# Kernel optimization log

Hardware: AMD Instinct MI355X
Metric: run time of the kernel (lower is better)

Reference implementation:

```python
import jax, jax.numpy as jnp
import numpy as np
from jax import lax

B, T, D, H, K = 2, 2048, 1024, 16, 4
HD = D // H           # head dim = 64
CONV_DIM = 3 * D      # q + k + v channels


def _l2norm(x, eps=1e-6):
    return x * lax.rsqrt(jnp.sum(x * x, axis=-1, keepdims=True) + eps)


def setup_inputs() -> dict:
    key = jax.random.key(0)
    ks = jax.random.split(key, 8)
    s = 0.02
    return {
        "x": jax.random.normal(ks[0], (B, T, D), jnp.float32),
        "W_qkv": jax.random.normal(ks[1], (CONV_DIM, D), jnp.float32) * s,
        "conv_w": jax.random.normal(ks[2], (CONV_DIM, 1, K), jnp.float32) * 0.25,
        "W_z": jax.random.normal(ks[3], (D, D), jnp.float32) * s,
        "W_b": jax.random.normal(ks[4], (H, D), jnp.float32) * s,
        "W_a": jax.random.normal(ks[5], (H, D), jnp.float32) * s,
        "dt_bias": jnp.ones((H,), jnp.float32),
        "A_log": jnp.log(jnp.arange(1, H + 1, dtype=jnp.float32)),
        "W_out": jax.random.normal(ks[6], (D, D), jnp.float32) * s,
    }


def _forward(x, W_qkv, conv_w, W_z, W_b, W_a, dt_bias, A_log, W_out):
    b_, t_, d_ = x.shape
    # fused qkv projection: [B,T,3D]
    mixed = jnp.einsum("btd,cd->btc", x, W_qkv)
    # causal depthwise conv1d (left pad K-1, truncate to T)
    c = mixed.transpose(0, 2, 1)  # [B,3D,T]
    c = lax.conv_general_dilated(
        c, conv_w, window_strides=(1,), padding=[(K - 1, 0)],
        dimension_numbers=("NCH", "OIH", "NCH"), feature_group_count=CONV_DIM)
    mixed = jax.nn.silu(c).transpose(0, 2, 1)  # [B,T,3D]

    q, k, v = jnp.split(mixed, [d_, 2 * d_], axis=-1)
    q = q.reshape(b_, t_, H, HD)
    k = k.reshape(b_, t_, H, HD)
    v = v.reshape(b_, t_, H, HD)

    z = jnp.einsum("btd,ed->bte", x, W_z).reshape(b_, t_, H, HD)
    beta = jax.nn.sigmoid(jnp.einsum("btd,hd->bth", x, W_b))          # [B,T,H]
    g = -jnp.exp(A_log) * jax.nn.softplus(
        jnp.einsum("btd,hd->bth", x, W_a) + dt_bias)                   # [B,T,H]

    q = _l2norm(q) * (HD ** -0.5)
    k = _l2norm(k)

    # sequential gated delta-rule scan over time
    qs = q.transpose(1, 0, 2, 3)       # [T,B,H,HD]
    ks_ = k.transpose(1, 0, 2, 3)
    vs = v.transpose(1, 0, 2, 3)
    bs = beta.transpose(1, 0, 2)       # [T,B,H]
    gs = g.transpose(1, 0, 2)

    def step(S, inp):
        q_t, k_t, v_t, b_t, g_t = inp
        S = S * jnp.exp(g_t)[..., None, None]                         # decay state
        S = S + jnp.einsum("bhd,bhv->bhdv", k_t, v_t * b_t[..., None])  # rank-1 update
        o_t = jnp.einsum("bhd,bhdv->bhv", q_t, S)
        return S, o_t

    S0 = jnp.zeros((b_, H, HD, HD), x.dtype)
    _, out = lax.scan(step, S0, (qs, ks_, vs, bs, gs))                 # out: [T,B,H,HD]
    out = out.transpose(1, 0, 2, 3)                                    # [B,T,H,HD]

    # gated RMSNorm over head dim, gate = silu(z)
    var = jnp.mean(out * out, axis=-1, keepdims=True)
    out = out * lax.rsqrt(var + 1e-6) * jax.nn.silu(z)

    out = out.reshape(b_, t_, d_)
    return jnp.einsum("btd,ed->bte", out, W_out)


def reference(x, W_qkv, conv_w, W_z, W_b, W_a, dt_bias, A_log, W_out):
    return _forward(x, W_qkv, conv_w, W_z, W_b, W_a, dt_bias, A_log, W_out)
```

## Files before the change

kernel.cpp:

```cpp
#include <hip/hip_runtime.h>
#include <math.h>

#define B_  2
#define T_  2048
#define D_  1024
#define H_  16
#define HD_ 64
#define CD_ 3072
#define L_  64
#define NC_ 32
#define TS  72
#define TT  8

typedef __attribute__((ext_vector_type(8))) short bf16x8;
typedef __attribute__((ext_vector_type(4))) float f32x4;
typedef __attribute__((ext_vector_type(4))) unsigned short u16x4;

__device__ __forceinline__ unsigned short f2bf(float f) {
    unsigned int u = __float_as_uint(f);
    unsigned int r = (u + 0x7fffu + ((u >> 16) & 1u)) >> 16;
    return (unsigned short)r;
}
__device__ __forceinline__ float bf2f(unsigned short u) {
    return __uint_as_float(((unsigned int)u) << 16);
}

__global__ __launch_bounds__(256)
void cvt_all(const float* __restrict__ x, const float* __restrict__ Wqkv,
             const float* __restrict__ Wz, const float* __restrict__ Wout,
             unsigned short* __restrict__ xb, unsigned short* __restrict__ Wqkvb,
             unsigned short* __restrict__ Wzb, unsigned short* __restrict__ Woutb) {
    int i = blockIdx.x * 256 + threadIdx.x;
    const float* src; unsigned short* dst; int li;
    if (i < 1048576)      { src = x;    dst = xb;    li = i; }
    else if (i < 1835008) { src = Wqkv; dst = Wqkvb; li = i - 1048576; }
    else if (i < 2097152) { src = Wz;   dst = Wzb;   li = i - 1835008; }
    else                  { src = Wout; dst = Woutb; li = i - 2097152; }
    float4 a = ((const float4*)src)[li];
    u16x4 o;
    o.x = f2bf(a.x); o.y = f2bf(a.y); o.z = f2bf(a.z); o.w = f2bf(a.w);
    ((u16x4*)dst)[li] = o;
}

__global__ __launch_bounds__(512, 2)
void gemm_qkvz256(const unsigned short* __restrict__ A,
                  const unsigned short* __restrict__ Bw,
                  unsigned short* __restrict__ mixedb, unsigned short* __restrict__ zb) {
    const int K = 1024;
    extern __shared__ short lds[];
    const int tid = threadIdx.x;
    const int bm = (blockIdx.x >> 4) * 256;
    const int bn = (blockIdx.x & 15) * 256;
    const int wid = tid >> 6;
    const int lane = tid & 63;
    const int wm = (wid >> 2) * 128;
    const int wn = (wid & 3) * 64;
    const int lr = lane & 15;
    const int lk = lane >> 4;

    f32x4 acc[8][4] = {};

    const int srow = tid >> 3;
    const int sphys = tid & 7;
    const int sgcol = ((sphys ^ (srow & 7)) << 3);
    const unsigned short* Ag = A + (size_t)(bm + srow) * K + sgcol;
    const unsigned short* Bg = Bw + (size_t)(bn + srow) * K + sgcol;
    short* ldsAd = lds + srow * 64 + sphys * 8;
    short* ldsBd = ldsAd + 16384;

#define SA2(bsel, kt, j0)                                                        \
    do {                                                                         \
        _Pragma("unroll")                                                        \
        for (int jj = (j0); jj < (j0) + 2; ++jj)                                 \
            __builtin_amdgcn_global_load_lds(                                    \
                (const __attribute__((address_space(1))) void*)(Ag + (size_t)(jj * 64) * K + (kt) * 64), \
                (__attribute__((address_space(3))) void*)(ldsAd + (bsel) * 32768 + jj * 4096), 16, 0, 0); \
    } while (0)
#define SB2(bsel, kt, j0)                                                        \
    do {                                                                         \
        _Pragma("unroll")                                                        \
        for (int jj = (j0); jj < (j0) + 2; ++jj)                                 \
            __builtin_amdgcn_global_load_lds(                                    \
                (const __attribute__((address_space(1))) void*)(Bg + (size_t)(jj * 64) * K + (kt) * 64), \
                (__attribute__((address_space(3))) void*)(ldsBd + (bsel) * 32768 + jj * 4096), 16, 0, 0); \
    } while (0)

    SA2(0, 0, 0); SB2(0, 0, 0); SA2(0, 0, 2); SB2(0, 0, 2);

    for (int kt = 0; kt < 16; ++kt) {
        const int cur = kt & 1;
        const int nb = cur ^ 1;
        asm volatile("s_waitcnt vmcnt(0)" ::: "memory");
        __builtin_amdgcn_sched_barrier(0);
        __builtin_amdgcn_s_barrier();
        const short* LA = lds + cur * 32768 + (wm + lr) * 64;
        const short* LB = lds + cur * 32768 + 16384 + (wn + lr) * 64;
        bf16x8 bf[4], af[4];
        const int ch0 = (lk ^ (lr & 7)) * 8;
        const int ch1 = ((4 + lk) ^ (lr & 7)) * 8;

#pragma unroll
        for (int ni = 0; ni < 4; ++ni) bf[ni] = *(const bf16x8*)(LB + ni * 1024 + ch0);
#pragma unroll
        for (int mi = 0; mi < 4; ++mi) af[mi] = *(const bf16x8*)(LA + mi * 1024 + ch0);
        if (kt < 15) SA2(nb, kt + 1, 0);
        __builtin_amdgcn_s_setprio(1);
#pragma unroll
        for (int mi = 0; mi < 4; ++mi)
#pragma unroll
            for (int ni = 0; ni < 4; ++ni)
                acc[mi][ni] = __builtin_amdgcn_mfma_f32_16x16x32_bf16(
                    af[mi], bf[ni], acc[mi][ni], 0, 0, 0);
        __builtin_amdgcn_s_setprio(0);
        __builtin_amdgcn_s_barrier();

#pragma unroll
        for (int mi = 0; mi < 4; ++mi) af[mi] = *(const bf16x8*)(LA + (mi + 4) * 1024 + ch0);
        if (kt < 15) SB2(nb, kt + 1, 0);
        __builtin_amdgcn_s_setprio(1);
#pragma unroll
        for (int mi = 0; mi < 4; ++mi)
#pragma unroll
            for (int ni = 0; ni < 4; ++ni)
                acc[mi + 4][ni] = __builtin_amdgcn_mfma_f32_16x16x32_bf16(
                    af[mi], bf[ni], acc[mi + 4][ni], 0, 0, 0);
        __builtin_amdgcn_s_setprio(0);
        __builtin_amdgcn_s_barrier();

#pragma unroll
        for (int ni = 0; ni < 4; ++ni) bf[ni] = *(const bf16x8*)(LB + ni * 1024 + ch1);
#pragma unroll
        for (int mi = 0; mi < 4; ++mi) af[mi] = *(const bf16x8*)(LA + mi * 1024 + ch1);
        if (kt < 15) SA2(nb, kt + 1, 2);
        __builtin_amdgcn_s_setprio(1);
#pragma unroll
        for (int mi = 0; mi < 4; ++mi)
#pragma unroll
            for (int ni = 0; ni < 4; ++ni)
                acc[mi][ni] = __builtin_amdgcn_mfma_f32_16x16x32_bf16(
                    af[mi], bf[ni], acc[mi][ni], 0, 0, 0);
        __builtin_amdgcn_s_setprio(0);
        __builtin_amdgcn_s_barrier();

#pragma unroll
        for (int mi = 0; mi < 4; ++mi) af[mi] = *(const bf16x8*)(LA + (mi + 4) * 1024 + ch1);
        if (kt < 15) SB2(nb, kt + 1, 2);
        __builtin_amdgcn_s_setprio(1);
#pragma unroll
        for (int mi = 0; mi < 4; ++mi)
#pragma unroll
            for (int ni = 0; ni < 4; ++ni)
                acc[mi + 4][ni] = __builtin_amdgcn_mfma_f32_16x16x32_bf16(
                    af[mi], bf[ni], acc[mi + 4][ni], 0, 0, 0);
        __builtin_amdgcn_s_setprio(0);
        __builtin_amdgcn_s_barrier();
    }

    const int r0 = lk * 4;
#pragma unroll
    for (int mi = 0; mi < 8; ++mi)
#pragma unroll
        for (int ni = 0; ni < 4; ++ni) {
            int row = bm + wm + mi * 16 + r0;
            int col = bn + wn + ni * 16 + lr;
            if (bn < 3072) {
                unsigned short* cp = mixedb + (size_t)row * 3072 + col;
#pragma unroll
                for (int r = 0; r < 4; ++r) cp[(size_t)r * 3072] = f2bf(acc[mi][ni][r]);
            } else {
                unsigned short* cp = zb + (size_t)row * 1024 + (col - 3072);
#pragma unroll
                for (int r = 0; r < 4; ++r) cp[(size_t)r * 1024] = f2bf(acc[mi][ni][r]);
            }
        }
}

__global__ __launch_bounds__(256, 2)
void gemm_out(const unsigned short* __restrict__ A,
              const unsigned short* __restrict__ Bw,
              float* __restrict__ C) {
    const int K = 1024, N = 1024;
    __shared__ short Ls[2][16384];
    const int tid = threadIdx.x;
    const int bm = (blockIdx.x >> 3) * 128;
    const int bn = (blockIdx.x & 7) * 128;
    const int wave = tid >> 6;
    const int lane = tid & 63;
    const int wm = (wave >> 1) * 64;
    const int wn = (wave & 1) * 64;
    const int lr = lane & 15;
    const int lk = lane >> 4;

    f32x4 acc[4][4] = {};

    const int srow = tid >> 3;
    const int sphys = tid & 7;
    const int sgcol = ((sphys ^ (srow & 7)) << 3);
    const unsigned short* Ag = A + (size_t)(bm + srow) * K + sgcol;
    const unsigned short* Bg = Bw + (size_t)(bn + srow) * K + sgcol;
    short* ldsAd = &Ls[0][0] + srow * 64 + sphys * 8;
    short* ldsBd = ldsAd + 8192;

#define STG_O(bsel, kt)                                                          \
    do {                                                                         \
        _Pragma("unroll")                                                        \
        for (int j = 0; j < 4; ++j) {                                            \
            __builtin_amdgcn_global_load_lds(                                    \
                (const __attribute__((address_space(1))) void*)(Ag + (size_t)(j * 32) * K + (kt) * 64), \
                (__attribute__((address_space(3))) void*)(ldsAd + (bsel) * 16384 + j * 2048), 16, 0, 0); \
            __builtin_amdgcn_global_load_lds(                                    \
                (const __attribute__((address_space(1))) void*)(Bg + (size_t)(j * 32) * K + (kt) * 64), \
                (__attribute__((address_space(3))) void*)(ldsBd + (bsel) * 16384 + j * 2048), 16, 0, 0); \
        }                                                                        \
    } while (0)

#define CMP_O(bsel)                                                              \
    do {                                                                         \
        const short* LA = &Ls[bsel][0] + (wm + lr) * 64;                         \
        const short* LB = &Ls[bsel][8192] + (wn + lr) * 64;                      \
        _Pragma("unroll")                                                        \
        for (int ks = 0; ks < 2; ++ks) {                                         \
            const int ch = ((ks * 4 + lk) ^ (lr & 7)) * 8;                       \
            bf16x8 af[4], bf[4];                                                 \
            _Pragma("unroll")                                                    \
            for (int mi = 0; mi < 4; ++mi) af[mi] = *(const bf16x8*)(LA + mi * 1024 + ch); \
            _Pragma("unroll")                                                    \
            for (int ni = 0; ni < 4; ++ni) bf[ni] = *(const bf16x8*)(LB + ni * 1024 + ch); \
            __builtin_amdgcn_s_setprio(1);                                       \
            _Pragma("unroll")                                                    \
            for (int mi = 0; mi < 4; ++mi)                                       \
                _Pragma("unroll")                                                \
                for (int ni = 0; ni < 4; ++ni)                                   \
                    acc[mi][ni] = __builtin_amdgcn_mfma_f32_16x16x32_bf16(       \
                        af[mi], bf[ni], acc[mi][ni], 0, 0, 0);                   \
            __builtin_amdgcn_s_setprio(0);                                       \
        }                                                                        \
    } while (0)

    STG_O(0, 0);
    __syncthreads();
    for (int kt = 0; kt < 15; ++kt) {
        STG_O((kt + 1) & 1, kt + 1);
        CMP_O(kt & 1);
        __syncthreads();
    }
    CMP_O(1);

    const int r0 = lk * 4;
#pragma unroll
    for (int mi = 0; mi < 4; ++mi)
#pragma unroll
        for (int ni = 0; ni < 4; ++ni) {
            float* cp = C + (size_t)(bm + wm + mi * 16 + r0) * N + bn + wn + ni * 16 + lr;
#pragma unroll
            for (int r = 0; r < 4; ++r)
                cp[(size_t)r * N] = acc[mi][ni][r];
        }
}

#define PJS 129
__global__ __launch_bounds__(256)
void proj_bg_partial(const float* __restrict__ x, const float* __restrict__ Wb,
                     const float* __restrict__ Wa, float* __restrict__ partial) {
    const int m0 = (blockIdx.x >> 3) * 32;
    const int ks = blockIdx.x & 7;
    const int k0 = ks * 128;
    const int tid = threadIdx.x;
    __shared__ float xs[32 * PJS];
    __shared__ float wsh[32 * PJS];
    const int sr = tid >> 3;
    const int sc = (tid & 7) << 4;
    const int mi2 = tid >> 3;
    const int n02 = (tid & 7) << 2;

    {
        const float* xrow = x + (size_t)(m0 + sr) * D_ + k0 + sc;
        const float* wrow = ((sr < 16) ? (Wb + (size_t)sr * D_) : (Wa + (size_t)(sr - 16) * D_)) + k0 + sc;
#pragma unroll
        for (int j = 0; j < 16; j += 4) {
            float4 a = *(const float4*)(xrow + j);
            float4 b = *(const float4*)(wrow + j);
            xs[sr * PJS + sc + j + 0] = a.x; xs[sr * PJS + sc + j + 1] = a.y;
            xs[sr * PJS + sc + j + 2] = a.z; xs[sr * PJS + sc + j + 3] = a.w;
            wsh[sr * PJS + sc + j + 0] = b.x; wsh[sr * PJS + sc + j + 1] = b.y;
            wsh[sr * PJS + sc + j + 2] = b.z; wsh[sr * PJS + sc + j + 3] = b.w;
        }
    }
    __syncthreads();

    float acc[4] = {0.f, 0.f, 0.f, 0.f};
#pragma unroll 8
    for (int kk = 0; kk < 128; ++kk) {
        float av = xs[mi2 * PJS + kk];
#pragma unroll
        for (int j = 0; j < 4; ++j)
            acc[j] = fmaf(av, wsh[(n02 + j) * PJS + kk], acc[j]);
    }
    float* op = partial + (size_t)ks * (4096 * 32) + (size_t)(m0 + mi2) * 32 + n02;
    *(float4*)op = make_float4(acc[0], acc[1], acc[2], acc[3]);
}

__global__ __launch_bounds__(256)
void proj_bg_reduce(const float* __restrict__ partial, const float* __restrict__ dt_bias,
                    const float* __restrict__ A_log,
                    float* __restrict__ beta, float* __restrict__ g) {
    const int gid = blockIdx.x * 256 + threadIdx.x;
    const int m = gid >> 5;
    const int n = gid & 31;
    float s = 0.f;
#pragma unroll
    for (int ks = 0; ks < 8; ++ks)
        s += partial[(size_t)ks * (4096 * 32) + gid];
    if (n < 16) {
        beta[(size_t)m * H_ + n] = 1.f / (1.f + expf(-s));
    } else {
        int h = n - 16;
        float spin = s + dt_bias[h];
        float sp = (spin > 20.f) ? spin : log1pf(expf(spin));
        g[(size_t)m * H_ + h] = -expf(A_log[h]) * sp;
    }
}

__global__ __launch_bounds__(256)
void conv_silu_tt(const unsigned short* __restrict__ mixedb,
                  const float* __restrict__ conv_w,
                  unsigned short* __restrict__ qkvb) {
    int idx = blockIdx.x * 256 + threadIdx.x;
    const int cq = idx % (CD_ / 4);
    const int bt8 = idx / (CD_ / 4);
    const int t0 = (bt8 % (T_ / TT)) * TT;
    const int b = bt8 / (T_ / TT);
    const int c0 = cq << 2;
    const unsigned short* base = mixedb + (size_t)(b * T_ + t0) * CD_ + c0;

    float vals[TT + 3][4];
#pragma unroll
    for (int i = 0; i < TT + 3; ++i) {
        int t = t0 + i - 3;
        if (t >= 0) {
            u16x4 m = *(const u16x4*)(base + (ptrdiff_t)(i - 3) * CD_);
            vals[i][0] = bf2f(m.x); vals[i][1] = bf2f(m.y);
            vals[i][2] = bf2f(m.z); vals[i][3] = bf2f(m.w);
        } else {
            vals[i][0] = vals[i][1] = vals[i][2] = vals[i][3] = 0.f;
        }
    }
    const float4* wp = (const float4*)(conv_w + (size_t)c0 * 4);
    float4 w[4] = {wp[0], wp[1], wp[2], wp[3]};

    unsigned short* outp = qkvb + (size_t)(b * T_ + t0) * CD_ + c0;
#pragma unroll
    for (int tt = 0; tt < TT; ++tt) {
        u16x4 r;
        float s0 = vals[tt + 3][0] * w[0].w + vals[tt + 2][0] * w[0].z
                 + vals[tt + 1][0] * w[0].y + vals[tt + 0][0] * w[0].x;
        float s1 = vals[tt + 3][1] * w[1].w + vals[tt + 2][1] * w[1].z
                 + vals[tt + 1][1] * w[1].y + vals[tt + 0][1] * w[1].x;
        float s2 = vals[tt + 3][2] * w[2].w + vals[tt + 2][2] * w[2].z
                 + vals[tt + 1][2] * w[2].y + vals[tt + 0][2] * w[2].x;
        float s3 = vals[tt + 3][3] * w[3].w + vals[tt + 2][3] * w[3].z
                 + vals[tt + 1][3] * w[3].y + vals[tt + 0][3] * w[3].x;
        r.x = f2bf(s0 / (1.f + expf(-s0)));
        r.y = f2bf(s1 / (1.f + expf(-s1)));
        r.z = f2bf(s2 / (1.f + expf(-s2)));
        r.w = f2bf(s3 / (1.f + expf(-s3)));
        *(u16x4*)(outp + (size_t)tt * CD_) = r;
    }
}

__global__ __launch_bounds__(256)
void chunk_phase1(const unsigned short* __restrict__ qkvb,
                  const float* __restrict__ beta, const float* __restrict__ gg,
                  float* __restrict__ dST, float* __restrict__ cum,
                  float* __restrict__ ac) {
    const int cid = blockIdx.x;
    const int c = cid & (NC_ - 1);
    const int bh = cid >> 5;
    const int b = bh >> 4, h = bh & 15;
    const int tid = threadIdx.x;
    const int wave = tid >> 6, lane = tid & 63;
    const int t0 = c * L_;

    __shared__ __align__(16) short kT[64 * TS];
    __shared__ __align__(16) short vT[64 * TS];
    __shared__ float cumS[64], wS[64];
    __shared__ float ksumP[4][64];

    const unsigned short* rowp = qkvb + (size_t)(b * T_ + t0 + lane) * CD_ + h * HD_ + wave * 16;
    bf16x8 k0 = *(const bf16x8*)(rowp + D_);
    bf16x8 k1 = *(const bf16x8*)(rowp + D_ + 8);
    bf16x8 v0 = *(const bf16x8*)(rowp + 2 * D_);
    bf16x8 v1 = *(const bf16x8*)(rowp + 2 * D_ + 8);

    {
        float ks = 0.f;
#pragma unroll
        for (int j = 0; j < 8; ++j) {
            float a = bf2f((unsigned short)k0[j]); ks = fmaf(a, a, ks);
            float bq = bf2f((unsigned short)k1[j]); ks = fmaf(bq, bq, ks);
        }
        ksumP[wave][lane] = ks;
    }

    if (wave == 0) {
        float s = gg[(size_t)(b * T_ + t0 + lane) * H_ + h];
#pragma unroll
        for (int off = 1; off < 64; off <<= 1) {
            float up = __shfl_up(s, off, 64);
            if (lane >= off) s += up;
        }
        cumS[lane] = s;
        float cend = __shfl(s, 63, 64);
        wS[lane] = expf(cend - s) * beta[(size_t)(b * T_ + t0 + lane) * H_ + h];
        cum[(size_t)bh * T_ + t0 + lane] = s;
        if (lane == 63) ac[cid] = expf(cend);
    }
    __syncthreads();
    const float kn = rsqrtf(ksumP[0][lane] + ksumP[1][lane] + ksumP[2][lane]
                            + ksumP[3][lane] + 1e-6f);
    const float w = wS[lane] * kn;
#pragma unroll
    for (int j = 0; j < 8; ++j) {
        kT[(wave * 16 + j) * TS + lane] = k0[j];
        kT[(wave * 16 + 8 + j) * TS + lane] = k1[j];
        vT[(wave * 16 + j) * TS + lane] = f2bf(bf2f((unsigned short)v0[j]) * w);
        vT[(wave * 16 + 8 + j) * TS + lane] = f2bf(bf2f((unsigned short)v1[j]) * w);
    }
    __syncthreads();

    const int lr = lane & 15, lk = lane >> 4;
    f32x4 acc[4] = {};
    const short* pA = vT + (wave * 16 + lr) * TS + lk * 8;
#pragma unroll
    for (int kk = 0; kk < 2; ++kk) {
        bf16x8 a = *(const bf16x8*)(pA + kk * 32);
#pragma unroll
        for (int n = 0; n < 4; ++n) {
            bf16x8 bfr = *(const bf16x8*)(kT + (n * 16 + lr) * TS + lk * 8 + kk * 32);
            acc[n] = __builtin_amdgcn_mfma_f32_16x16x32_bf16(a, bfr, acc[n], 0, 0, 0);
        }
    }
#pragma unroll
    for (int n = 0; n < 4; ++n) {
        float* op = dST + (size_t)cid * 4096 + (wave * 16 + lk * 4) * 64 + n * 16 + lr;
#pragma unroll
        for (int r = 0; r < 4; ++r)
            op[r * 64] = acc[n][r];
    }
}

__global__ __launch_bounds__(256)
void chunk_phase2(float* __restrict__ dST, const float* __restrict__ ac) {
    const int gid = blockIdx.x * 256 + threadIdx.x;
    const int bh = gid >> 12;
    const int e = gid & 4095;
    float s = 0.f;
    for (int c = 0; c < NC_; ++c) {
        size_t off = (size_t)(bh * NC_ + c) * 4096 + e;
        float tmp = dST[off];
        dST[off] = s;
        s = fmaf(ac[bh * NC_ + c], s, tmp);
    }
}

__global__ __launch_bounds__(256)
void chunk_phase3(const unsigned short* __restrict__ qkvb,
                  const float* __restrict__ beta, const float* __restrict__ cum,
                  const float* __restrict__ states,
                  const unsigned short* __restrict__ zb,
                  unsigned short* __restrict__ normb) {
    const int cid = blockIdx.x;
    const int c = cid & (NC_ - 1);
    const int bh = cid >> 5;
    const int b = bh >> 4, h = bh & 15;
    const int tid = threadIdx.x;
    const int wave = tid >> 6, lane = tid & 63;
    const int t0 = c * L_;

    __shared__ __align__(16) short vT[64 * TS];
    __shared__ __align__(16) short sT[64 * TS];
    __shared__ __align__(16) short pS[64 * TS];
    __shared__ float cumS[64], betaS[64];
    __shared__ float invq[64], invk[64];

    {
        const unsigned short* rowp = qkvb + (size_t)(b * T_ + t0 + lane) * CD_ + 2 * D_ + h * HD_ + wave * 16;
        bf16x8 v0 = *(const bf16x8*)rowp;
        bf16x8 v1 = *(const bf16x8*)(rowp + 8);
#pragma unroll
        for (int j = 0; j < 8; ++j) {
            vT[(wave * 16 + j) * TS + lane] = v0[j];
            vT[(wave * 16 + 8 + j) * TS + lane] = v1[j];
        }
    }
    {
        const float* sp = states + (size_t)cid * 4096 + (tid >> 2) * 64 + (tid & 3) * 16;
        short* dp = sT + (tid >> 2) * TS + (tid & 3) * 16;
#pragma unroll
        for (int j = 0; j < 16; j += 4) {
            float4 f = *(const float4*)(sp + j);
            dp[j] = f2bf(f.x); dp[j + 1] = f2bf(f.y);
            dp[j + 2] = f2bf(f.z); dp[j + 3] = f2bf(f.w);
        }
    }
    {
        int row = tid >> 2;
        int seg = (tid & 3) << 4;
        const unsigned short* qr = qkvb + (size_t)(b * T_ + t0 + row) * CD_ + h * HD_ + seg;
        bf16x8 a0 = *(const bf16x8*)qr;
        bf16x8 a1 = *(const bf16x8*)(qr + 8);
        float sq = 0.f;
#pragma unroll
        for (int j = 0; j < 8; ++j) {
            float v = bf2f((unsigned short)a0[j]); sq = fmaf(v, v, sq);
            v = bf2f((unsigned short)a1[j]); sq = fmaf(v, v, sq);
        }
        sq += __shfl_xor(sq, 1, 64);
        sq += __shfl_xor(sq, 2, 64);
        const unsigned short* kr = qr + D_;
        bf16x8 b0 = *(const bf16x8*)kr;
        bf16x8 b1 = *(const bf16x8*)(kr + 8);
        float sk = 0.f;
#pragma unroll
        for (int j = 0; j < 8; ++j) {
            float v = bf2f((unsigned short)b0[j]); sk = fmaf(v, v, sk);
            v = bf2f((unsigned short)b1[j]); sk = fmaf(v, v, sk);
        }
        sk += __shfl_xor(sk, 1, 64);
        sk += __shfl_xor(sk, 2, 64);
        if ((tid & 3) == 0) {
            invq[row] = 0.125f * rsqrtf(sq + 1e-6f);
            invk[row] = rsqrtf(sk + 1e-6f);
        }
    }
    if (tid < 64) {
        cumS[tid] = cum[(size_t)bh * T_ + t0 + tid];
        betaS[tid] = beta[(size_t)(b * T_ + t0 + tid) * H_ + h];
    }
    __syncthreads();

    const int lr = lane & 15, lk = lane >> 4;
    const unsigned short* qrow = qkvb + (size_t)(b * T_ + t0 + wave * 16 + lr) * CD_ + h * HD_;
    bf16x8 qf0 = *(const bf16x8*)(qrow + lk * 8);
    bf16x8 qf1 = *(const bf16x8*)(qrow + 32 + lk * 8);

    f32x4 pacc[4] = {};
#pragma unroll
    for (int n = 0; n < 4; ++n) {
        const unsigned short* krow = qkvb + (size_t)(b * T_ + t0 + n * 16 + lr) * CD_ + D_ + h * HD_;
        bf16x8 b0 = *(const bf16x8*)(krow + lk * 8);
        bf16x8 b1 = *(const bf16x8*)(krow + 32 + lk * 8);
        pacc[n] = __builtin_amdgcn_mfma_f32_16x16x32_bf16(qf0, b0, pacc[n], 0, 0, 0);
        pacc[n] = __builtin_amdgcn_mfma_f32_16x16x32_bf16(qf1, b1, pacc[n], 0, 0, 0);
    }
#pragma unroll
    for (int n = 0; n < 4; ++n) {
        int s = n * 16 + lr;
        float cs = cumS[s], bsk = betaS[s] * invk[s];
#pragma unroll
        for (int r = 0; r < 4; ++r) {
            int t = wave * 16 + lk * 4 + r;
            float pv = (s <= t) ? expf(cumS[t] - cs) * bsk * pacc[n][r] * invq[t] : 0.f;
            pS[t * TS + s] = f2bf(pv);
        }
    }
    __syncthreads();

    f32x4 oacc[4] = {};
#pragma unroll
    for (int n = 0; n < 4; ++n) {
        const short* srow = sT + (n * 16 + lr) * TS + lk * 8;
        bf16x8 b0 = *(const bf16x8*)srow;
        bf16x8 b1 = *(const bf16x8*)(srow + 32);
        oacc[n] = __builtin_amdgcn_mfma_f32_16x16x32_bf16(qf0, b0, oacc[n], 0, 0, 0);
        oacc[n] = __builtin_amdgcn_mfma_f32_16x16x32_bf16(qf1, b1, oacc[n], 0, 0, 0);
    }
    float qsc[4];
#pragma unroll
    for (int r = 0; r < 4; ++r) {
        int t = wave * 16 + lk * 4 + r;
        qsc[r] = expf(cumS[t]) * invq[t];
    }
#pragma unroll
    for (int n = 0; n < 4; ++n)
#pragma unroll
        for (int r = 0; r < 4; ++r) oacc[n][r] *= qsc[r];
    const short* prow = pS + (wave * 16 + lr) * TS + lk * 8;
    bf16x8 pf0 = *(const bf16x8*)prow;
    bf16x8 pf1 = *(const bf16x8*)(prow + 32);
#pragma unroll
    for (int n = 0; n < 4; ++n) {
        const short* vrow = vT + (n * 16 + lr) * TS + lk * 8;
        bf16x8 b0 = *(const bf16x8*)vrow;
        bf16x8 b1 = *(const bf16x8*)(vrow + 32);
        oacc[n] = __builtin_amdgcn_mfma_f32_16x16x32_bf16(pf0, b0, oacc[n], 0, 0, 0);
        oacc[n] = __builtin_amdgcn_mfma_f32_16x16x32_bf16(pf1, b1, oacc[n], 0, 0, 0);
    }

#pragma unroll
    for (int r = 0; r < 4; ++r) {
        int t = wave * 16 + lk * 4 + r;
        float ss = 0.f;
#pragma unroll
        for (int n = 0; n < 4; ++n) ss = fmaf(oacc[n][r], oacc[n][r], ss);
        ss += __shfl_xor(ss, 1, 64);
        ss += __shfl_xor(ss, 2, 64);
        ss += __shfl_xor(ss, 4, 64);
        ss += __shfl_xor(ss, 8, 64);
        float inv = rsqrtf(ss * (1.f / 64.f) + 1e-6f);
        size_t rowoff = (size_t)(b * T_ + t0 + t) * D_ + h * HD_;
#pragma unroll
        for (int n = 0; n < 4; ++n) {
            float zv = bf2f(zb[rowoff + n * 16 + lr]);
            float sz = zv / (1.f + expf(-zv));
            normb[rowoff + n * 16 + lr] = f2bf(oacc[n][r] * inv * sz);
        }
    }
}

extern "C" void kernel_launch(void* const* d_in, const int* in_sizes, int n_in,
                              void* d_out, int out_size, void* d_ws, size_t ws_size,
                              hipStream_t stream) {
    const float* x       = (const float*)d_in[0];
    const float* W_qkv   = (const float*)d_in[1];
    const float* conv_w  = (const float*)d_in[2];
    const float* W_z     = (const float*)d_in[3];
    const float* W_b     = (const float*)d_in[4];
    const float* W_a     = (const float*)d_in[5];
    const float* dt_bias = (const float*)d_in[6];
    const float* A_log   = (const float*)d_in[7];
    const float* W_out   = (const float*)d_in[8];
    float* out = (float*)d_out;

    float* ws = (float*)d_ws;
    unsigned short* mixedb = (unsigned short*)ws;
    float* dST    = ws;
    unsigned short* normb = (unsigned short*)(ws + 4194304);
    float* betab  = ws + 8388608;
    float* gb     = ws + 8454144;
    float* cum    = ws + 8519680;
    float* ac     = ws + 8585216;
    unsigned short* Woutb = (unsigned short*)(ws + 8586240);
    unsigned short* xb    = (unsigned short*)(ws + 12582912);
    unsigned short* Wqkvb = (unsigned short*)(ws + 14680064);
    unsigned short* Wzb   = (unsigned short*)(ws + 16252928);
    unsigned short* qkvb  = (unsigned short*)(ws + 12582912);
    unsigned short* zb    = (unsigned short*)(ws + 18874368);
    float* bgpart = ws + 23068672;

    const int M = B_ * T_;
    dim3 blk(256);

    cvt_all<<<dim3(9216), blk, 0, stream>>>(x, W_qkv, W_z, W_out, xb, Wqkvb, Wzb, Woutb);

    gemm_qkvz256<<<dim3(256), dim3(512), 131072, stream>>>(xb, Wqkvb, mixedb, zb);

    conv_silu_tt<<<dim3(B_ * (T_ / TT) * (CD_ / 4) / 256), blk, 0, stream>>>(mixedb, conv_w, qkvb);

    proj_bg_partial<<<dim3(1024), blk, 0, stream>>>(x, W_b, W_a, bgpart);
    proj_bg_reduce<<<dim3(512), blk, 0, stream>>>(bgpart, dt_bias, A_log, betab, gb);

    chunk_phase1<<<dim3(B_ * H_ * NC_), blk, 0, stream>>>(qkvb, betab, gb, dST, cum, ac);
    chunk_phase2<<<dim3(B_ * H_ * 4096 / 256), blk, 0, stream>>>(dST, ac);
    chunk_phase3<<<dim3(B_ * H_ * NC_), blk, 0, stream>>>(qkvb, betab, cum, dST, zb, normb);

    gemm_out<<<dim3(256), blk, 0, stream>>>(normb, Woutb, out);
}
```

Before: 134.0 us.

## Fuse causal conv+SiLU and beta/g reduction into chunk phase kernels

Removes the standalone conv_silu_tt and proj_bg_reduce kernels. Chunk phase1 and phase3 now load the raw projected rows, compute the depthwise causal conv and SiLU on the fly, and phase1 also reduces the beta/g partial sums itself. Phase3 stages q and k in shared memory and computes the norms from them. This drops two launches and the round trip of the qkv intermediate through global memory. In exchange, conv work is recomputed in both phases and each output row now needs four input rows of loads. The workspace layout is reshuffled to fit.

```diff
diff --git a/kernel.cpp b/kernel.cpp
--- a/kernel.cpp
+++ b/kernel.cpp
@@ -10,7 +10,6 @@
 #define L_  64
 #define NC_ 32
 #define TS  72
-#define TT  8
 
 typedef __attribute__((ext_vector_type(8))) short bf16x8;
 typedef __attribute__((ext_vector_type(4))) float f32x4;
@@ -301,78 +300,12 @@
 }
 
 __global__ __launch_bounds__(256)
-void proj_bg_reduce(const float* __restrict__ partial, const float* __restrict__ dt_bias,
-                    const float* __restrict__ A_log,
-                    float* __restrict__ beta, float* __restrict__ g) {
-    const int gid = blockIdx.x * 256 + threadIdx.x;
-    const int m = gid >> 5;
-    const int n = gid & 31;
-    float s = 0.f;
-#pragma unroll
-    for (int ks = 0; ks < 8; ++ks)
-        s += partial[(size_t)ks * (4096 * 32) + gid];
-    if (n < 16) {
-        beta[(size_t)m * H_ + n] = 1.f / (1.f + expf(-s));
-    } else {
-        int h = n - 16;
-        float spin = s + dt_bias[h];
-        float sp = (spin > 20.f) ? spin : log1pf(expf(spin));
-        g[(size_t)m * H_ + h] = -expf(A_log[h]) * sp;
-    }
-}
-
-__global__ __launch_bounds__(256)
-void conv_silu_tt(const unsigned short* __restrict__ mixedb,
+void chunk_phase1(const unsigned short* __restrict__ mixedb,
                   const float* __restrict__ conv_w,
-                  unsigned short* __restrict__ qkvb) {
-    int idx = blockIdx.x * 256 + threadIdx.x;
-    const int cq = idx % (CD_ / 4);
-    const int bt8 = idx / (CD_ / 4);
-    const int t0 = (bt8 % (T_ / TT)) * TT;
-    const int b = bt8 / (T_ / TT);
-    const int c0 = cq << 2;
-    const unsigned short* base = mixedb + (size_t)(b * T_ + t0) * CD_ + c0;
-
-    float vals[TT + 3][4];
-#pragma unroll
-    for (int i = 0; i < TT + 3; ++i) {
-        int t = t0 + i - 3;
-        if (t >= 0) {
-            u16x4 m = *(const u16x4*)(base + (ptrdiff_t)(i - 3) * CD_);
-            vals[i][0] = bf2f(m.x); vals[i][1] = bf2f(m.y);
-            vals[i][2] = bf2f(m.z); vals[i][3] = bf2f(m.w);
-        } else {
-            vals[i][0] = vals[i][1] = vals[i][2] = vals[i][3] = 0.f;
-        }
-    }
-    const float4* wp = (const float4*)(conv_w + (size_t)c0 * 4);
-    float4 w[4] = {wp[0], wp[1], wp[2], wp[3]};
-
-    unsigned short* outp = qkvb + (size_t)(b * T_ + t0) * CD_ + c0;
-#pragma unroll
-    for (int tt = 0; tt < TT; ++tt) {
-        u16x4 r;
-        float s0 = vals[tt + 3][0] * w[0].w + vals[tt + 2][0] * w[0].z
-                 + vals[tt + 1][0] * w[0].y + vals[tt + 0][0] * w[0].x;
-        float s1 = vals[tt + 3][1] * w[1].w + vals[tt + 2][1] * w[1].z
-                 + vals[tt + 1][1] * w[1].y + vals[tt + 0][1] * w[1].x;
-        float s2 = vals[tt + 3][2] * w[2].w + vals[tt + 2][2] * w[2].z
-                 + vals[tt + 1][2] * w[2].y + vals[tt + 0][2] * w[2].x;
-        float s3 = vals[tt + 3][3] * w[3].w + vals[tt + 2][3] * w[3].z
-                 + vals[tt + 1][3] * w[3].y + vals[tt + 0][3] * w[3].x;
-        r.x = f2bf(s0 / (1.f + expf(-s0)));
-        r.y = f2bf(s1 / (1.f + expf(-s1)));
-        r.z = f2bf(s2 / (1.f + expf(-s2)));
-        r.w = f2bf(s3 / (1.f + expf(-s3)));
-        *(u16x4*)(outp + (size_t)tt * CD_) = r;
-    }
-}
-
-__global__ __launch_bounds__(256)
-void chunk_phase1(const unsigned short* __restrict__ qkvb,
-                  const float* __restrict__ beta, const float* __restrict__ gg,
+                  const float* __restrict__ bgpart,
+                  const float* __restrict__ dt_bias, const float* __restrict__ A_log,
                   float* __restrict__ dST, float* __restrict__ cum,
-                  float* __restrict__ ac) {
+                  float* __restrict__ ac, float* __restrict__ betab) {
     const int cid = blockIdx.x;
     const int c = cid & (NC_ - 1);
     const int bh = cid >> 5;
@@ -386,24 +319,62 @@
     __shared__ float cumS[64], wS[64];
     __shared__ float ksumP[4][64];
 
-    const unsigned short* rowp = qkvb + (size_t)(b * T_ + t0 + lane) * CD_ + h * HD_ + wave * 16;
-    bf16x8 k0 = *(const bf16x8*)(rowp + D_);
-    bf16x8 k1 = *(const bf16x8*)(rowp + D_ + 8);
-    bf16x8 v0 = *(const bf16x8*)(rowp + 2 * D_);
-    bf16x8 v1 = *(const bf16x8*)(rowp + 2 * D_ + 8);
-
-    {
-        float ks = 0.f;
+    const int colk = D_ + h * HD_ + wave * 16;
+    const int tloc = t0 + lane;
+    const bf16x8 zz = {0, 0, 0, 0, 0, 0, 0, 0};
+    bf16x8 kr[4][2], vr[4][2];
+#pragma unroll
+    for (int ri = 0; ri < 4; ++ri) {
+        int tt = tloc - 3 + ri;
+        if (tt >= 0) {
+            const unsigned short* bp = mixedb + (size_t)(b * T_ + tt) * CD_ + colk;
+            kr[ri][0] = *(const bf16x8*)bp;
+            kr[ri][1] = *(const bf16x8*)(bp + 8);
+            vr[ri][0] = *(const bf16x8*)(bp + D_);
+            vr[ri][1] = *(const bf16x8*)(bp + D_ + 8);
+        } else {
+            kr[ri][0] = zz; kr[ri][1] = zz; vr[ri][0] = zz; vr[ri][1] = zz;
+        }
+    }
+    unsigned short kb[16], vb[16];
+    float ksq = 0.f;
+#pragma unroll
+    for (int half = 0; half < 2; ++half)
 #pragma unroll
         for (int j = 0; j < 8; ++j) {
-            float a = bf2f((unsigned short)k0[j]); ks = fmaf(a, a, ks);
-            float bq = bf2f((unsigned short)k1[j]); ks = fmaf(bq, bq, ks);
-        }
-        ksumP[wave][lane] = ks;
-    }
+            int ch = colk + half * 8 + j;
+            float4 wk = *(const float4*)(conv_w + (size_t)ch * 4);
+            float sk = bf2f((unsigned short)kr[3][half][j]) * wk.w
+                     + bf2f((unsigned short)kr[2][half][j]) * wk.z
+                     + bf2f((unsigned short)kr[1][half][j]) * wk.y
+                     + bf2f((unsigned short)kr[0][half][j]) * wk.x;
+            sk = sk / (1.f + expf(-sk));
+            unsigned short kbi = f2bf(sk);
+            kb[half * 8 + j] = kbi;
+            float kf = bf2f(kbi);
+            ksq = fmaf(kf, kf, ksq);
+            float4 wv = *(const float4*)(conv_w + (size_t)(ch + D_) * 4);
+            float sv = bf2f((unsigned short)vr[3][half][j]) * wv.w
+                     + bf2f((unsigned short)vr[2][half][j]) * wv.z
+                     + bf2f((unsigned short)vr[1][half][j]) * wv.y
+                     + bf2f((unsigned short)vr[0][half][j]) * wv.x;
+            sv = sv / (1.f + expf(-sv));
+            vb[half * 8 + j] = f2bf(sv);
+        }
+    ksumP[wave][lane] = ksq;
 
     if (wave == 0) {
-        float s = gg[(size_t)(b * T_ + t0 + lane) * H_ + h];
+        const int m = b * T_ + t0 + lane;
+        float sb = 0.f, sg = 0.f;
+#pragma unroll
+        for (int p = 0; p < 8; ++p) {
+            sb += bgpart[(size_t)p * 131072 + m * 32 + h];
+            sg += bgpart[(size_t)p * 131072 + m * 32 + 16 + h];
+        }
+        float bet = 1.f / (1.f + expf(-sb));
+        float spin = sg + dt_bias[h];
+        float sp = (spin > 20.f) ? spin : log1pf(expf(spin));
+        float s = -expf(A_log[h]) * sp;
 #pragma unroll
         for (int off = 1; off < 64; off <<= 1) {
             float up = __shfl_up(s, off, 64);
@@ -411,8 +382,9 @@
         }
         cumS[lane] = s;
         float cend = __shfl(s, 63, 64);
-        wS[lane] = expf(cend - s) * beta[(size_t)(b * T_ + t0 + lane) * H_ + h];
+        wS[lane] = expf(cend - s) * bet;
         cum[(size_t)bh * T_ + t0 + lane] = s;
+        betab[(size_t)m * H_ + h] = bet;
         if (lane == 63) ac[cid] = expf(cend);
     }
     __syncthreads();
@@ -420,11 +392,9 @@
                             + ksumP[3][lane] + 1e-6f);
     const float w = wS[lane] * kn;
 #pragma unroll
-    for (int j = 0; j < 8; ++j) {
-        kT[(wave * 16 + j) * TS + lane] = k0[j];
-        kT[(wave * 16 + 8 + j) * TS + lane] = k1[j];
-        vT[(wave * 16 + j) * TS + lane] = f2bf(bf2f((unsigned short)v0[j]) * w);
-        vT[(wave * 16 + 8 + j) * TS + lane] = f2bf(bf2f((unsigned short)v1[j]) * w);
+    for (int j = 0; j < 16; ++j) {
+        kT[(wave * 16 + j) * TS + lane] = (short)kb[j];
+        vT[(wave * 16 + j) * TS + lane] = (short)f2bf(bf2f(vb[j]) * w);
     }
     __syncthreads();
 
@@ -464,8 +434,9 @@
 }
 
 __global__ __launch_bounds__(256)
-void chunk_phase3(const unsigned short* __restrict__ qkvb,
-                  const float* __restrict__ beta, const float* __restrict__ cum,
+void chunk_phase3(const unsigned short* __restrict__ mixedb,
+                  const float* __restrict__ conv_w,
+                  const float* __restrict__ betab, const float* __restrict__ cum,
                   const float* __restrict__ states,
                   const unsigned short* __restrict__ zb,
                   unsigned short* __restrict__ normb) {
@@ -477,21 +448,103 @@
     const int wave = tid >> 6, lane = tid & 63;
     const int t0 = c * L_;
 
+    __shared__ __align__(16) short qS[64 * TS];
+    __shared__ __align__(16) short kS[64 * TS];
     __shared__ __align__(16) short vT[64 * TS];
     __shared__ __align__(16) short sT[64 * TS];
     __shared__ __align__(16) short pS[64 * TS];
     __shared__ float cumS[64], betaS[64];
     __shared__ float invq[64], invk[64];
+    __shared__ float qsumP[4][64], ksumP[4][64];
+
+    const int colq = h * HD_ + wave * 16;
+    const int tloc = t0 + lane;
+    const bf16x8 zz = {0, 0, 0, 0, 0, 0, 0, 0};
 
     {
-        const unsigned short* rowp = qkvb + (size_t)(b * T_ + t0 + lane) * CD_ + 2 * D_ + h * HD_ + wave * 16;
-        bf16x8 v0 = *(const bf16x8*)rowp;
-        bf16x8 v1 = *(const bf16x8*)(rowp + 8);
-#pragma unroll
-        for (int j = 0; j < 8; ++j) {
-            vT[(wave * 16 + j) * TS + lane] = v0[j];
-            vT[(wave * 16 + 8 + j) * TS + lane] = v1[j];
-        }
+        bf16x8 r[4][2];
+#pragma unroll
+        for (int ri = 0; ri < 4; ++ri) {
+            int tt = tloc - 3 + ri;
+            if (tt >= 0) {
+                const unsigned short* bp = mixedb + (size_t)(b * T_ + tt) * CD_ + colq;
+                r[ri][0] = *(const bf16x8*)bp;
+                r[ri][1] = *(const bf16x8*)(bp + 8);
+            } else { r[ri][0] = zz; r[ri][1] = zz; }
+        }
+        float sq = 0.f;
+#pragma unroll
+        for (int half = 0; half < 2; ++half)
+#pragma unroll
+            for (int j = 0; j < 8; ++j) {
+                int ch = colq + half * 8 + j;
+                float4 w4 = *(const float4*)(conv_w + (size_t)ch * 4);
+                float s = bf2f((unsigned short)r[3][half][j]) * w4.w
+                        + bf2f((unsigned short)r[2][half][j]) * w4.z
+                        + bf2f((unsigned short)r[1][half][j]) * w4.y
+                        + bf2f((unsigned short)r[0][half][j]) * w4.x;
+                s = s / (1.f + expf(-s));
+                unsigned short ub = f2bf(s);
+                qS[lane * TS + wave * 16 + half * 8 + j] = (short)ub;
+                float f = bf2f(ub);
+                sq = fmaf(f, f, sq);
+            }
+        qsumP[wave][lane] = sq;
+    }
+    {
+        bf16x8 r[4][2];
+#pragma unroll
+        for (int ri = 0; ri < 4; ++ri) {
+            int tt = tloc - 3 + ri;
+            if (tt >= 0) {
+                const unsigned short* bp = mixedb + (size_t)(b * T_ + tt) * CD_ + D_ + colq;
+                r[ri][0] = *(const bf16x8*)bp;
+                r[ri][1] = *(const bf16x8*)(bp + 8);
+            } else { r[ri][0] = zz; r[ri][1] = zz; }
+        }
+        float sk = 0.f;
+#pragma unroll
+        for (int half = 0; half < 2; ++half)
+#pragma unroll
+            for (int j = 0; j < 8; ++j) {
+                int ch = D_ + colq + half * 8 + j;
+                float4 w4 = *(const float4*)(conv_w + (size_t)ch * 4);
+                float s = bf2f((unsigned short)r[3][half][j]) * w4.w
+                        + bf2f((unsigned short)r[2][half][j]) * w4.z
+                        + bf2f((unsigned short)r[1][half][j]) * w4.y
+                        + bf2f((unsigned short)r[0][half][j]) * w4.x;
+                s = s / (1.f + expf(-s));
+                unsigned short ub = f2bf(s);
+                kS[lane * TS + wave * 16 + half * 8 + j] = (short)ub;
+                float f = bf2f(ub);
+                sk = fmaf(f, f, sk);
+            }
+        ksumP[wave][lane] = sk;
+    }
+    {
+        bf16x8 r[4][2];
+#pragma unroll
+        for (int ri = 0; ri < 4; ++ri) {
+            int tt = tloc - 3 + ri;
+            if (tt >= 0) {
+                const unsigned short* bp = mixedb + (size_t)(b * T_ + tt) * CD_ + 2 * D_ + colq;
+                r[ri][0] = *(const bf16x8*)bp;
+                r[ri][1] = *(const bf16x8*)(bp + 8);
+            } else { r[ri][0] = zz; r[ri][1] = zz; }
+        }
+#pragma unroll
+        for (int half = 0; half < 2; ++half)
+#pragma unroll
+            for (int j = 0; j < 8; ++j) {
+                int ch = 2 * D_ + colq + half * 8 + j;
+                float4 w4 = *(const float4*)(conv_w + (size_t)ch * 4);
+                float s = bf2f((unsigned short)r[3][half][j]) * w4.w
+                        + bf2f((unsigned short)r[2][half][j]) * w4.z
+                        + bf2f((unsigned short)r[1][half][j]) * w4.y
+                        + bf2f((unsigned short)r[0][half][j]) * w4.x;
+                s = s / (1.f + expf(-s));
+                vT[(wave * 16 + half * 8 + j) * TS + lane] = (short)f2bf(s);
+            }
     }
     {
         const float* sp = states + (size_t)cid * 4096 + (tid >> 2) * 64 + (tid & 3) * 16;
@@ -503,56 +556,34 @@
             dp[j + 2] = f2bf(f.z); dp[j + 3] = f2bf(f.w);
         }
     }
-    {
-        int row = tid >> 2;
-        int seg = (tid & 3) << 4;
-        const unsigned short* qr = qkvb + (size_t)(b * T_ + t0 + row) * CD_ + h * HD_ + seg;
-        bf16x8 a0 = *(const bf16x8*)qr;
-        bf16x8 a1 = *(const bf16x8*)(qr + 8);
-        float sq = 0.f;
-#pragma unroll
-        for (int j = 0; j < 8; ++j) {
-            float v = bf2f((unsigned short)a0[j]); sq = fmaf(v, v, sq);
-            v = bf2f((unsigned short)a1[j]); sq = fmaf(v, v, sq);
-        }
-        sq += __shfl_xor(sq, 1, 64);
-        sq += __shfl_xor(sq, 2, 64);
-        const unsigned short* kr = qr + D_;
-        bf16x8 b0 = *(const bf16x8*)kr;
-        bf16x8 b1 = *(const bf16x8*)(kr + 8);
-        float sk = 0.f;
-#pragma unroll
-        for (int j = 0; j < 8; ++j) {
-            float v = bf2f((unsigned short)b0[j]); sk = fmaf(v, v, sk);
-            v = bf2f((unsigned short)b1[j]); sk = fmaf(v, v, sk);
-        }
-        sk += __shfl_xor(sk, 1, 64);
-        sk += __shfl_xor(sk, 2, 64);
-        if ((tid & 3) == 0) {
-            invq[row] = 0.125f * rsqrtf(sq + 1e-6f);
-            invk[row] = rsqrtf(sk + 1e-6f);
-        }
-    }
     if (tid < 64) {
         cumS[tid] = cum[(size_t)bh * T_ + t0 + tid];
-        betaS[tid] = beta[(size_t)(b * T_ + t0 + tid) * H_ + h];
+        betaS[tid] = betab[(size_t)(b * T_ + t0 + tid) * H_ + h];
     }
     __syncthreads();
 
+    if (tid < 64) {
+        invq[tid] = 0.125f * rsqrtf(qsumP[0][tid] + qsumP[1][tid] + qsumP[2][tid]
+                                    + qsumP[3][tid] + 1e-6f);
+        invk[tid] = rsqrtf(ksumP[0][tid] + ksumP[1][tid] + ksumP[2][tid]
+                           + ksumP[3][tid] + 1e-6f);
+    }
+
     const int lr = lane & 15, lk = lane >> 4;
-    const unsigned short* qrow = qkvb + (size_t)(b * T_ + t0 + wave * 16 + lr) * CD_ + h * HD_;
-    bf16x8 qf0 = *(const bf16x8*)(qrow + lk * 8);
-    bf16x8 qf1 = *(const bf16x8*)(qrow + 32 + lk * 8);
+    bf16x8 qf0 = *(const bf16x8*)(qS + (wave * 16 + lr) * TS + lk * 8);
+    bf16x8 qf1 = *(const bf16x8*)(qS + (wave * 16 + lr) * TS + 32 + lk * 8);
 
     f32x4 pacc[4] = {};
 #pragma unroll
     for (int n = 0; n < 4; ++n) {
-        const unsigned short* krow = qkvb + (size_t)(b * T_ + t0 + n * 16 + lr) * CD_ + D_ + h * HD_;
-        bf16x8 b0 = *(const bf16x8*)(krow + lk * 8);
-        bf16x8 b1 = *(const bf16x8*)(krow + 32 + lk * 8);
+        const short* krow = kS + (n * 16 + lr) * TS + lk * 8;
+        bf16x8 b0 = *(const bf16x8*)krow;
+        bf16x8 b1 = *(const bf16x8*)(krow + 32);
         pacc[n] = __builtin_amdgcn_mfma_f32_16x16x32_bf16(qf0, b0, pacc[n], 0, 0, 0);
         pacc[n] = __builtin_amdgcn_mfma_f32_16x16x32_bf16(qf1, b1, pacc[n], 0, 0, 0);
     }
+    __syncthreads();
+
 #pragma unroll
     for (int n = 0; n < 4; ++n) {
         int s = n * 16 + lr;
@@ -634,35 +665,31 @@
 
     float* ws = (float*)d_ws;
     unsigned short* mixedb = (unsigned short*)ws;
-    float* dST    = ws;
-    unsigned short* normb = (unsigned short*)(ws + 4194304);
+    unsigned short* normb  = (unsigned short*)(ws + 6291456);
     float* betab  = ws + 8388608;
-    float* gb     = ws + 8454144;
-    float* cum    = ws + 8519680;
-    float* ac     = ws + 8585216;
-    unsigned short* Woutb = (unsigned short*)(ws + 8586240);
+    float* cum    = ws + 8454144;
+    float* ac     = ws + 8519680;
+    unsigned short* Woutb = (unsigned short*)(ws + 8520704);
     unsigned short* xb    = (unsigned short*)(ws + 12582912);
     unsigned short* Wqkvb = (unsigned short*)(ws + 14680064);
     unsigned short* Wzb   = (unsigned short*)(ws + 16252928);
-    unsigned short* qkvb  = (unsigned short*)(ws + 12582912);
-    unsigned short* zb    = (unsigned short*)(ws + 18874368);
+    unsigned short* zb    = (unsigned short*)(ws + 16777216);
+    float* dST    = ws + 18874368;
     float* bgpart = ws + 23068672;
 
-    const int M = B_ * T_;
     dim3 blk(256);
 
     cvt_all<<<dim3(9216), blk, 0, stream>>>(x, W_qkv, W_z, W_out, xb, Wqkvb, Wzb, Woutb);
 
     gemm_qkvz256<<<dim3(256), dim3(512), 131072, stream>>>(xb, Wqkvb, mixedb, zb);
 
-    conv_silu_tt<<<dim3(B_ * (T_ / TT) * (CD_ / 4) / 256), blk, 0, stream>>>(mixedb, conv_w, qkvb);
-
     proj_bg_partial<<<dim3(1024), blk, 0, stream>>>(x, W_b, W_a, bgpart);
-    proj_bg_reduce<<<dim3(512), blk, 0, stream>>>(bgpart, dt_bias, A_log, betab, gb);
-
-    chunk_phase1<<<dim3(B_ * H_ * NC_), blk, 0, stream>>>(qkvb, betab, gb, dST, cum, ac);
+
+    chunk_phase1<<<dim3(B_ * H_ * NC_), blk, 0, stream>>>(
+        mixedb, conv_w, bgpart, dt_bias, A_log, dST, cum, ac, betab);
     chunk_phase2<<<dim3(B_ * H_ * 4096 / 256), blk, 0, stream>>>(dST, ac);
-    chunk_phase3<<<dim3(B_ * H_ * NC_), blk, 0, stream>>>(qkvb, betab, cum, dST, zb, normb);
+    chunk_phase3<<<dim3(B_ * H_ * NC_), blk, 0, stream>>>(
+        mixedb, conv_w, betab, cum, dST, zb, normb);
 
     gemm_out<<<dim3(256), blk, 0, stream>>>(normb, Woutb, out);
 }
```

After: 146.3 us. 1.09x slower.
